# Kernel tuning notes

Hardware: AMD Instinct MI355X
Metric: run time of the kernel (lower is better)

Reference implementation:

```python
import jax, jax.numpy as jnp
import numpy as np

C = 256
GROUPS = 32
EPS = 1e-5

def setup_inputs() -> dict:
    key = jax.random.key(0)
    ks = jax.random.split(key, 7)
    B, H, W = 4, 64, 64
    x = jax.random.normal(ks[0], (B, C, H, W), dtype=jnp.float32)
    # GroupNorm affine params
    gn_w = jnp.ones((C,), dtype=jnp.float32)
    gn_b = jnp.zeros((C,), dtype=jnp.float32)
    # 1x1 conv weights stored as [out, in]
    s = 1.0 / np.sqrt(C)
    qkv_w = jax.random.uniform(ks[1], (3 * C, C), minval=-s, maxval=s, dtype=jnp.float32)
    qkv_b = jax.random.uniform(ks[2], (3 * C,), minval=-s, maxval=s, dtype=jnp.float32)
    proj_w = jax.random.uniform(ks[3], (C, C), minval=-s, maxval=s, dtype=jnp.float32)
    proj_b = jax.random.uniform(ks[4], (C,), minval=-s, maxval=s, dtype=jnp.float32)
    return {"x": x, "gn_w": gn_w, "gn_b": gn_b, "qkv_w": qkv_w,
            "qkv_b": qkv_b, "proj_w": proj_w, "proj_b": proj_b}

def group_norm(x, w, b):
    B, Cc, H, W = x.shape
    xg = x.reshape(B, GROUPS, Cc // GROUPS, H, W)
    mu = xg.mean(axis=(2, 3, 4), keepdims=True)
    var = xg.var(axis=(2, 3, 4), keepdims=True)
    xn = ((xg - mu) * jax.lax.rsqrt(var + EPS)).reshape(B, Cc, H, W)
    return xn * w[None, :, None, None] + b[None, :, None, None]

def reference(x, gn_w, gn_b, qkv_w, qkv_b, proj_w, proj_b):
    B, Cc, H, W = x.shape
    h = group_norm(x, gn_w, gn_b)
    # 1x1 conv == per-pixel matmul
    qkv = jnp.einsum('bchw,oc->bohw', h, qkv_w) + qkv_b[None, :, None, None]
    q, k, v = jnp.split(qkv, 3, axis=1)            # each [B, C, H, W]
    N = H * W
    q = q.reshape(B, Cc, N).transpose(0, 2, 1)      # [B, N, C]
    k = k.reshape(B, Cc, N)                         # [B, C, N]
    v = v.reshape(B, Cc, N).transpose(0, 2, 1)      # [B, N, C]
    w_att = jnp.einsum('bnc,bcm->bnm', q, k) * (Cc ** -0.5)
    w_att = jax.nn.softmax(w_att, axis=-1)
    h = jnp.einsum('bnm,bmc->bnc', w_att, v)        # [B, N, C]
    h = h.transpose(0, 2, 1).reshape(B, Cc, H, W)
    h = jnp.einsum('bchw,oc->bohw', h, proj_w) + proj_b[None, :, None, None]
    return x + h
```

## Files before the change

kernel.cpp:

```cpp
#include <hip/hip_runtime.h>
#include <stdint.h>

typedef unsigned short u16;
typedef __attribute__((ext_vector_type(8))) short bf16x8;
typedef __attribute__((ext_vector_type(4))) float f32x4;

#define BATCH   4
#define CH      256
#define NPIX    4096
#define NGROUPS 32
#define CPG     8
#define EPS     1e-5f

#define NSPLIT 4
#define SPLEN  (NPIX / NSPLIT)
#define ATK    32
#define NIT    (SPLEN / ATK)
#define WSTR   264
#define QTILES 2

__device__ __forceinline__ float bf2f(u16 u) {
    union { uint32_t i; float f; } v; v.i = ((uint32_t)u) << 16; return v.f;
}
__device__ __forceinline__ u16 f2bf(float f) {
    union { float f; uint32_t i; } v; v.f = f;
    uint32_t x = v.i;
    uint32_t r = (x + 0x7fffu + ((x >> 16) & 1u)) >> 16;
    return (u16)r;
}
__device__ __forceinline__ void unpack2(uint32_t u, float& a, float& b) {
    union { uint32_t i; float f; } lo, hi;
    lo.i = u << 16; hi.i = u & 0xffff0000u;
    a = lo.f; b = hi.f;
}
__device__ __forceinline__ void unpack8(uint4 u, float* f) {
    unpack2(u.x, f[0], f[1]); unpack2(u.y, f[2], f[3]);
    unpack2(u.z, f[4], f[5]); unpack2(u.w, f[6], f[7]);
}

__device__ __forceinline__ bool detect_f32(const void* xv) {
    const u16* p = (const u16*)xv;
    int bad = 0;
    #pragma unroll
    for (int i = 0; i < 32; i++) {
        u16 v = p[2 * i];
        int e = (v >> 7) & 0xff;
        bad += (e < 0x68 || e > 0x90) ? 1 : 0;
    }
    return bad >= 10;
}
__device__ __forceinline__ float load1(const void* b, size_t i, bool f32) {
    return f32 ? ((const float*)b)[i] : bf2f(((const u16*)b)[i]);
}
__device__ __forceinline__ void store1(void* b, size_t i, bool f32, float v) {
    if (f32) ((float*)b)[i] = v; else ((u16*)b)[i] = f2bf(v);
}
__device__ __forceinline__ void load4v(const void* base, size_t off, bool f32, float* f) {
    if (f32) {
        float4 a = *(const float4*)((const float*)base + off);
        f[0] = a.x; f[1] = a.y; f[2] = a.z; f[3] = a.w;
    } else {
        uint2 u = *(const uint2*)((const u16*)base + off);
        unpack2(u.x, f[0], f[1]); unpack2(u.y, f[2], f[3]);
    }
}
__device__ __forceinline__ void load8v(const void* base, size_t off, bool f32, float* f) {
    if (f32) {
        const float4* p = (const float4*)((const float*)base + off);
        float4 a = p[0], b = p[1];
        f[0] = a.x; f[1] = a.y; f[2] = a.z; f[3] = a.w;
        f[4] = b.x; f[5] = b.y; f[6] = b.z; f[7] = b.w;
    } else {
        uint4 u = *(const uint4*)((const u16*)base + off);
        unpack8(u, f);
    }
}

__global__ __launch_bounds__(256) void wconv(const void* __restrict__ qkv_w,
                                             const void* __restrict__ proj_w,
                                             u16* __restrict__ wq, u16* __restrict__ wp) {
    bool f32q = detect_f32(qkv_w);
    bool f32p = detect_f32(proj_w);
    int i = blockIdx.x * 256 + threadIdx.x;
    for (int e = i; e < 768 * 256; e += 256 * 256)
        wq[e] = f2bf(load1(qkv_w, e, f32q));
    for (int e = i; e < 256 * 256; e += 256 * 256)
        wp[e] = f2bf(load1(proj_w, e, f32p));
}

__global__ __launch_bounds__(256) void gn_stats(const void* __restrict__ x,
                                                float* __restrict__ stats, int b0) {
    bool f32 = detect_f32(x);
    int bg = b0 * NGROUPS + blockIdx.x;
    int t  = threadIdx.x;
    size_t base = (size_t)bg * (CPG * NPIX);
    float s = 0.f, s2 = 0.f;
    for (int i = t * 8; i < CPG * NPIX; i += 256 * 8) {
        float f[8]; load8v(x, base + i, f32, f);
        #pragma unroll
        for (int e = 0; e < 8; e++) { s += f[e]; s2 += f[e] * f[e]; }
    }
    #pragma unroll
    for (int off = 1; off < 64; off <<= 1) {
        s  += __shfl_xor(s,  off);
        s2 += __shfl_xor(s2, off);
    }
    __shared__ float red[8];
    int w = t >> 6;
    if ((t & 63) == 0) { red[w * 2] = s; red[w * 2 + 1] = s2; }
    __syncthreads();
    if (t == 0) {
        float S  = red[0] + red[2] + red[4] + red[6];
        float S2 = red[1] + red[3] + red[5] + red[7];
        float n  = (float)(CPG * NPIX);
        float mu = S / n;
        float var = S2 / n - mu * mu;
        stats[bg * 2]     = mu;
        stats[bg * 2 + 1] = rsqrtf(var + EPS);
    }
}

__global__ __launch_bounds__(256) void xgn(const void* __restrict__ x,
                                           const void* __restrict__ gn_w,
                                           const void* __restrict__ gn_b,
                                           const float* __restrict__ stats,
                                           u16* __restrict__ xt, int b0) {
    bool f32 = detect_f32(x);
    __shared__ u16 T[64][72];
    int bl = blockIdx.z, bg = b0 + bl;
    int n0 = blockIdx.x * 64, c0 = blockIdx.y * 64;
    int t = threadIdx.x;
    int tc = t >> 4, tn = (t & 15) * 4;
    #pragma unroll
    for (int i = 0; i < 4; i++) {
        int cl = tc + i * 16;
        int c = c0 + cl;
        int g = c >> 3;
        float mu = stats[(bg * NGROUPS + g) * 2];
        float rs = stats[(bg * NGROUPS + g) * 2 + 1];
        float wv = load1(gn_w, c, f32) * rs;
        float bv = load1(gn_b, c, f32) - mu * wv;
        float a[4];
        load4v(x, ((size_t)(bg * CH + c)) * NPIX + n0 + tn, f32, a);
        #pragma unroll
        for (int j = 0; j < 4; j++) T[cl][tn + j] = f2bf(a[j] * wv + bv);
    }
    __syncthreads();
    #pragma unroll
    for (int i = 0; i < 2; i++) {
        int e = t + i * 256;
        int nl = e >> 3, cc = (e & 7) * 8;
        union { uint4 v; u16 s[8]; } pk;
        #pragma unroll
        for (int j = 0; j < 8; j++) pk.s[j] = T[cc + j][nl];
        *(uint4*)(xt + ((size_t)(bl * NPIX) + n0 + nl) * CH + c0 + cc) = pk.v;
    }
}

__global__ __launch_bounds__(256, 3) void qkv_mfma(const u16* __restrict__ xt,
                                                   const u16* __restrict__ wq,
                                                   const void* __restrict__ qkv_b,
                                                   u16* __restrict__ qk,
                                                   u16* __restrict__ vt) {
    __shared__ u16 Ws[64 * WSTR];
    __shared__ u16 T2b[128 * 72];
    bool f32b = detect_f32(qkv_b);
    int bl = blockIdx.z;
    int o0 = blockIdx.y * 64;
    int t = threadIdx.x;
    int w = t >> 6, lane = t & 63;
    int l15 = lane & 15, quad = lane >> 4;

    #pragma unroll
    for (int i = 0; i < 8; i++) {
        int e = t + i * 256;
        *(uint4*)(Ws + (e >> 5) * WSTR + (e & 31) * 8) =
            *(const uint4*)(wq + (size_t)(o0 + (e >> 5)) * CH + (e & 31) * 8);
    }
    __syncthreads();

    bool isv = (o0 >= 512);
    for (int tt = 0; tt < QTILES; tt++) {
        int n0 = (blockIdx.x * QTILES + tt) * 128;
        int pbase = n0 + w * 32;
        const u16* xa = xt + ((size_t)(bl * NPIX + pbase)) * CH;

        f32x4 acc[2][4];
        #pragma unroll
        for (int m = 0; m < 2; m++)
            #pragma unroll
            for (int n = 0; n < 4; n++)
                #pragma unroll
                for (int r = 0; r < 4; r++) acc[m][n][r] = 0.f;

        #pragma unroll
        for (int kc = 0; kc < 8; kc++) {
            bf16x8 a0 = *(const bf16x8*)(xa + (size_t)(l15) * CH + kc * 32 + quad * 8);
            bf16x8 a1 = *(const bf16x8*)(xa + (size_t)(16 + l15) * CH + kc * 32 + quad * 8);
            #pragma unroll
            for (int n = 0; n < 4; n++) {
                bf16x8 b = *(const bf16x8*)(Ws + (n * 16 + l15) * WSTR + kc * 32 + quad * 8);
                acc[0][n] = __builtin_amdgcn_mfma_f32_16x16x32_bf16(a0, b, acc[0][n], 0, 0, 0);
                acc[1][n] = __builtin_amdgcn_mfma_f32_16x16x32_bf16(a1, b, acc[1][n], 0, 0, 0);
            }
        }

        if (!isv) {
            __syncthreads();
            #pragma unroll
            for (int n = 0; n < 4; n++) {
                int o = o0 + n * 16 + l15;
                float bias = load1(qkv_b, o, f32b);
                #pragma unroll
                for (int m = 0; m < 2; m++)
                    #pragma unroll
                    for (int r = 0; r < 4; r++) {
                        int prow = w * 32 + m * 16 + quad * 4 + r;
                        T2b[prow * 72 + n * 16 + l15] = f2bf(acc[m][n][r] + bias);
                    }
            }
            __syncthreads();
            #pragma unroll
            for (int i = 0; i < 4; i++) {
                int e = t + i * 256;
                int p = e >> 3, c = (e & 7) * 8;
                uint4 v = *(const uint4*)(T2b + p * 72 + c);
                *(uint4*)(qk + ((size_t)(bl * NPIX + n0 + p)) * 512 + o0 + c) = v;
            }
        } else {
            #pragma unroll
            for (int n = 0; n < 4; n++) {
                int o = o0 + n * 16 + l15;
                float bias = load1(qkv_b, o, f32b);
                size_t rowb = ((size_t)(bl * CH + o - 512)) * NPIX + pbase;
                #pragma unroll
                for (int m = 0; m < 2; m++) {
                    union { uint2 v; u16 s[4]; } pk;
                    #pragma unroll
                    for (int r = 0; r < 4; r++) pk.s[r] = f2bf(acc[m][n][r] + bias);
                    *(uint2*)(vt + rowb + quad * 8 + m * 4) = pk.v;
                }
            }
        }
    }
}

__global__ __launch_bounds__(256, 2) void attn_mfma(const u16* __restrict__ qk,
                                                    const u16* __restrict__ vt,
                                                    u16* __restrict__ Opart,
                                                    float* __restrict__ lpart,
                                                    int NE, int NR) {
    __shared__ u16 Ks[2][ATK * 256];
    __shared__ u16 Vts[2][CH * 32];
    int bl    = blockIdx.z;
    int split = blockIdx.y;
    int q0    = blockIdx.x * 128;
    int t     = threadIdx.x;
    int w     = t >> 6, lane = t & 63;
    int l15   = lane & 15, quad = lane >> 4;

    const u16* qkb = qk + (size_t)bl * NPIX * 512;
    const u16* vtb = vt + (size_t)bl * CH * NPIX;
    int kvbase = split * SPLEN;

    bf16x8 qf[2][8];
    #pragma unroll
    for (int m = 0; m < 2; m++) {
        const u16* qrow = qkb + (size_t)(q0 + w * 32 + m * 16 + l15) * 512;
        #pragma unroll
        for (int kc = 0; kc < 8; kc++)
            qf[m][kc] = *(const bf16x8*)(qrow + kc * 32 + quad * 8);
    }
    f32x4 o[2][16];
    #pragma unroll
    for (int m = 0; m < 2; m++)
        #pragma unroll
        for (int i = 0; i < 16; i++)
            #pragma unroll
            for (int r = 0; r < 4; r++) o[m][i][r] = 0.f;
    float lsum[2] = {0.f, 0.f};
    const float scale = 0.0625f;
    int swz = l15 & 7;

    #pragma unroll
    for (int i = 0; i < 4; i++) {
        int g = t + i * 256;
        int row = g >> 5, pcol = g & 31;
        int lcol = pcol ^ (row & 7);
        __builtin_amdgcn_global_load_lds(
            (const void*)(qkb + (size_t)(kvbase + row) * 512 + 256 + lcol * 8),
            (void*)(&Ks[0][0] + (size_t)g * 8), 16, 0, 0);
    }
    #pragma unroll
    for (int i = 0; i < 4; i++) {
        int g = t + i * 256;
        int row = g >> 2, s = g & 3;
        __builtin_amdgcn_global_load_lds(
            (const void*)(vtb + (size_t)row * NPIX + kvbase + (s ^ (row & 3)) * 8),
            (void*)(&Vts[0][0] + (size_t)g * 8), 16, 0, 0);
    }
    __syncthreads();

    for (int it = 0; it < NIT; it++) {
        int cur = it & 1;
        if (it + 1 < NIT) {
            int kv1 = kvbase + (it + 1) * ATK;
            u16* KsB = &Ks[cur ^ 1][0];
            u16* VsB = &Vts[cur ^ 1][0];
            #pragma unroll
            for (int i = 0; i < 4; i++) {
                int g = t + i * 256;
                int row = g >> 5, pcol = g & 31;
                int lcol = pcol ^ (row & 7);
                __builtin_amdgcn_global_load_lds(
                    (const void*)(qkb + (size_t)(kv1 + row) * 512 + 256 + lcol * 8),
                    (void*)(KsB + (size_t)g * 8), 16, 0, 0);
            }
            #pragma unroll
            for (int i = 0; i < 4; i++) {
                int g = t + i * 256;
                int row = g >> 2, s = g & 3;
                __builtin_amdgcn_global_load_lds(
                    (const void*)(vtb + (size_t)row * NPIX + kv1 + (s ^ (row & 3)) * 8),
                    (void*)(VsB + (size_t)g * 8), 16, 0, 0);
            }
        }
        const u16* KsC = &Ks[cur][0];
        const u16* VsC = &Vts[cur][0];

        f32x4 sT[2][2];
        #pragma unroll
        for (int kt = 0; kt < 2; kt++)
            #pragma unroll
            for (int qt = 0; qt < 2; qt++)
                #pragma unroll
                for (int r = 0; r < 4; r++) sT[kt][qt][r] = 0.f;
        #pragma unroll
        for (int kc = 0; kc < 8; kc++) {
            int sc = (kc * 4 + quad) ^ swz;
            bf16x8 a0 = *(const bf16x8*)(KsC + l15 * 256 + sc * 8);
            bf16x8 a1 = *(const bf16x8*)(KsC + (16 + l15) * 256 + sc * 8);
            sT[0][0] = __builtin_amdgcn_mfma_f32_16x16x32_bf16(a0, qf[0][kc], sT[0][0], 0, 0, 0);
            sT[0][1] = __builtin_amdgcn_mfma_f32_16x16x32_bf16(a0, qf[1][kc], sT[0][1], 0, 0, 0);
            sT[1][0] = __builtin_amdgcn_mfma_f32_16x16x32_bf16(a1, qf[0][kc], sT[1][0], 0, 0, 0);
            sT[1][1] = __builtin_amdgcn_mfma_f32_16x16x32_bf16(a1, qf[1][kc], sT[1][1], 0, 0, 0);
        }

        bf16x8 pa[2];
        #pragma unroll
        for (int qt = 0; qt < 2; qt++) {
            union { bf16x8 v; u16 s[8]; } pk;
            float ls = 0.f;
            #pragma unroll
            for (int kt = 0; kt < 2; kt++)
                #pragma unroll
                for (int r = 0; r < 4; r++) {
                    float p = __expf(sT[kt][qt][r] * scale);
                    ls += p;
                    pk.s[kt * 4 + r] = f2bf(p);
                }
            lsum[qt] += ls;
            pa[qt] = pk.v;
        }

        #pragma unroll
        for (int dt = 0; dt < 16; dt++) {
            int row = dt * 16 + l15;
            bf16x8 vf = *(const bf16x8*)(VsC + row * 32 + (quad ^ (row & 3)) * 8);
            o[0][dt] = __builtin_amdgcn_mfma_f32_16x16x32_bf16(pa[0], vf, o[0][dt], 0, 0, 0);
            o[1][dt] = __builtin_amdgcn_mfma_f32_16x16x32_bf16(pa[1], vf, o[1][dt], 0, 0, 0);
        }

        __syncthreads();
    }

    size_t rowb = (size_t)bl * NPIX + q0 + w * 32;
    u16* op = Opart + (size_t)split * NE;
    #pragma unroll
    for (int qt = 0; qt < 2; qt++) {
        float v = lsum[qt];
        v += __shfl_xor(v, 16); v += __shfl_xor(v, 32);
        if (quad == 0)
            lpart[(size_t)split * NR + rowb + qt * 16 + l15] = v;
        #pragma unroll
        for (int dt = 0; dt < 16; dt++)
            #pragma unroll
            for (int r = 0; r < 4; r++)
                op[(rowb + qt * 16 + quad * 4 + r) * CH + dt * 16 + l15] = f2bf(o[qt][dt][r]);
    }
}

__global__ __launch_bounds__(256, 4) void proj_mfma(const u16* __restrict__ Opart,
                                                    const float* __restrict__ lpart,
                                                    const u16* __restrict__ wp,
                                                    const void* __restrict__ proj_b,
                                                    const void* __restrict__ x,
                                                    void* __restrict__ out,
                                                    int b0, int NE, int NR) {
    __shared__ u16 Ws[64 * WSTR];
    bool f32 = detect_f32(x);
    int bl = blockIdx.z, bg = b0 + bl;
    int n0 = blockIdx.x * 128, o0 = blockIdx.y * 64;
    int t = threadIdx.x;
    int w = t >> 6, lane = t & 63;
    int l15 = lane & 15, quad = lane >> 4;
    int pbase = n0 + w * 32;

    #pragma unroll
    for (int i = 0; i < 8; i++) {
        int e = t + i * 256;
        *(uint4*)(Ws + (e >> 5) * WSTR + (e & 31) * 8) =
            *(const uint4*)(wp + (size_t)(o0 + (e >> 5)) * CH + (e & 31) * 8);
    }
    __syncthreads();

    size_t rowg[2]; float invl[2];
    #pragma unroll
    for (int m = 0; m < 2; m++) {
        rowg[m] = (size_t)bl * NPIX + pbase + m * 16 + l15;
        float l = 0.f;
        #pragma unroll
        for (int s = 0; s < NSPLIT; s++) l += lpart[(size_t)s * NR + rowg[m]];
        invl[m] = 1.0f / l;
    }

    f32x4 acc[2][4];
    #pragma unroll
    for (int m = 0; m < 2; m++)
        #pragma unroll
        for (int n = 0; n < 4; n++)
            #pragma unroll
            for (int r = 0; r < 4; r++) acc[m][n][r] = 0.f;

    #pragma unroll
    for (int kc = 0; kc < 8; kc++) {
        bf16x8 afr[2];
        #pragma unroll
        for (int m = 0; m < 2; m++) {
            float f[8] = {0.f,0.f,0.f,0.f,0.f,0.f,0.f,0.f};
            #pragma unroll
            for (int s = 0; s < NSPLIT; s++) {
                bf16x8 v = *(const bf16x8*)(Opart + (size_t)s * NE + rowg[m] * CH + kc * 32 + quad * 8);
                #pragma unroll
                for (int j = 0; j < 8; j++) f[j] += bf2f((u16)v[j]);
            }
            bf16x8 a;
            #pragma unroll
            for (int j = 0; j < 8; j++) a[j] = (short)f2bf(f[j] * invl[m]);
            afr[m] = a;
        }
        #pragma unroll
        for (int n = 0; n < 4; n++) {
            bf16x8 b = *(const bf16x8*)(Ws + (n * 16 + l15) * WSTR + kc * 32 + quad * 8);
            acc[0][n] = __builtin_amdgcn_mfma_f32_16x16x32_bf16(afr[0], b, acc[0][n], 0, 0, 0);
            acc[1][n] = __builtin_amdgcn_mfma_f32_16x16x32_bf16(afr[1], b, acc[1][n], 0, 0, 0);
        }
    }

    __syncthreads();
    float4* T4 = (float4*)Ws;
    #pragma unroll
    for (int n = 0; n < 4; n++) {
        int o = o0 + n * 16 + l15;
        float bias = load1(proj_b, o, f32);
        #pragma unroll
        for (int m = 0; m < 2; m++) {
            float4 v;
            v.x = acc[m][n][0] + bias; v.y = acc[m][n][1] + bias;
            v.z = acc[m][n][2] + bias; v.w = acc[m][n][3] + bias;
            T4[(n * 16 + l15) * 33 + w * 8 + m * 4 + quad] = v;
        }
    }
    __syncthreads();
    const float* Tf = (const float*)Ws;
    if (f32) {
        #pragma unroll
        for (int i = 0; i < 8; i++) {
            int idx = t + i * 256;
            int row = idx >> 5, c4 = idx & 31;
            float4 v = T4[row * 33 + c4];
            size_t go = ((size_t)(bg * CH + o0 + row)) * NPIX + n0 + c4 * 4;
            float4 xr = *(const float4*)((const float*)x + go);
            v.x += xr.x; v.y += xr.y; v.z += xr.z; v.w += xr.w;
            *(float4*)((float*)out + go) = v;
        }
    } else {
        #pragma unroll
        for (int i = 0; i < 4; i++) {
            int idx = t + i * 256;
            int row = idx >> 4, c8 = idx & 15;
            size_t go = ((size_t)(bg * CH + o0 + row)) * NPIX + n0 + c8 * 8;
            uint4 xr = *(const uint4*)((const u16*)x + go);
            float xf[8]; unpack8(xr, xf);
            union { uint4 v; u16 s[8]; } pk;
            #pragma unroll
            for (int j = 0; j < 8; j++)
                pk.s[j] = f2bf(Tf[row * 132 + c8 * 8 + j] + xf[j]);
            *(uint4*)((u16*)out + go) = pk.v;
        }
    }
}

extern "C" void kernel_launch(void* const* d_in, const int* in_sizes, int n_in,
                              void* d_out, int out_size, void* d_ws, size_t ws_size,
                              hipStream_t stream) {
    const void* x      = d_in[0];
    const void* gn_w   = d_in[1];
    const void* gn_b   = d_in[2];
    const void* qkv_w  = d_in[3];
    const void* qkv_b  = d_in[4];
    const void* proj_w = d_in[5];
    const void* proj_b = d_in[6];

    char* ws = (char*)d_ws;
    float* stats = (float*)ws;
    u16* wq = (u16*)(ws + 1024);
    u16* wp = wq + 768 * 256;
    char* dyn = ws + 1024 + (768 * 256 + 256 * 256) * 2;

    const size_t per_batch = (size_t)NPIX * CH * 2
                           + (size_t)NPIX * 512 * 2
                           + (size_t)CH * NPIX * 2
                           + (size_t)NSPLIT * NPIX * CH * 2
                           + (size_t)NSPLIT * NPIX * 4;
    const size_t need_full = 1024 + 600 * 1024 + BATCH * per_batch;
    int nb = (ws_size >= need_full) ? BATCH : 1;

    u16* xt      = (u16*)dyn;
    u16* qk      = xt + (size_t)nb * NPIX * CH;
    u16* vt      = qk + (size_t)nb * NPIX * 512;
    u16* Opart   = vt + (size_t)nb * CH * NPIX;
    float* lpart = (float*)(Opart + (size_t)NSPLIT * nb * NPIX * CH);
    int NE = nb * NPIX * CH;
    int NR = nb * NPIX;

    wconv<<<dim3(256), 256, 0, stream>>>(qkv_w, proj_w, wq, wp);

    for (int b0 = 0; b0 < BATCH; b0 += nb) {
        gn_stats<<<dim3(nb * NGROUPS), 256, 0, stream>>>(x, stats, b0);
        xgn<<<dim3(NPIX / 64, CH / 64, nb), 256, 0, stream>>>(
            x, gn_w, gn_b, stats, xt, b0);
        qkv_mfma<<<dim3(NPIX / 128 / QTILES, 768 / 64, nb), 256, 0, stream>>>(
            xt, wq, qkv_b, qk, vt);
        attn_mfma<<<dim3(NPIX / 128, NSPLIT, nb), 256, 0, stream>>>(
            qk, vt, Opart, lpart, NE, NR);
        proj_mfma<<<dim3(NPIX / 128, CH / 64, nb), 256, 0, stream>>>(
            Opart, lpart, wp, proj_b, x, d_out, b0, NE, NR);
    }
}
```

Baseline: 208.8 us.

## Store V in MFMA fragment order and load it directly from global memory

The QKV kernel now writes V into a pre-tiled layout that matches the per-lane B-fragment order of the 16x16x32 MFMA. The attention kernel then reads each V fragment with a single 16-byte global load per lane, with no LDS staging. This drops the V LDS double buffer and its async copies, which frees LDS and cuts shared-memory traffic. In exchange, V loads are now synchronous global (L2) loads inside the inner loop and are no longer prefetched a stage ahead.

Result: slower. 300.2 us (+43.8%).

```diff
diff --git a/kernel.cpp b/kernel.cpp
--- a/kernel.cpp
+++ b/kernel.cpp
@@ -161,7 +161,7 @@
                                                    const u16* __restrict__ wq,
                                                    const void* __restrict__ qkv_b,
                                                    u16* __restrict__ qk,
-                                                   u16* __restrict__ vt) {
+                                                   u16* __restrict__ vbuf) {
     __shared__ u16 Ws[64 * WSTR];
     __shared__ u16 T2b[128 * 72];
     bool f32b = detect_f32(qkv_b);
@@ -232,13 +232,15 @@
             for (int n = 0; n < 4; n++) {
                 int o = o0 + n * 16 + l15;
                 float bias = load1(qkv_b, o, f32b);
-                size_t rowb = ((size_t)(bl * CH + o - 512)) * NPIX + pbase;
+                int dt = ((o0 - 512) >> 4) + n;
+                size_t tb = ((size_t)(bl * 128 + (pbase >> 5)) * 16 + dt) * 512;
                 #pragma unroll
                 for (int m = 0; m < 2; m++) {
                     union { uint2 v; u16 s[4]; } pk;
                     #pragma unroll
                     for (int r = 0; r < 4; r++) pk.s[r] = f2bf(acc[m][n][r] + bias);
-                    *(uint2*)(vt + rowb + quad * 8 + m * 4) = pk.v;
+                    *(uint2*)(vbuf + tb + ((m + 2 * (quad & 1)) * 16 + l15) * 8
+                                     + 4 * (quad >> 1)) = pk.v;
                 }
             }
         }
@@ -246,12 +248,11 @@
 }
 
 __global__ __launch_bounds__(256, 2) void attn_mfma(const u16* __restrict__ qk,
-                                                    const u16* __restrict__ vt,
+                                                    const u16* __restrict__ vbuf,
                                                     u16* __restrict__ Opart,
                                                     float* __restrict__ lpart,
                                                     int NE, int NR) {
     __shared__ u16 Ks[2][ATK * 256];
-    __shared__ u16 Vts[2][CH * 32];
     int bl    = blockIdx.z;
     int split = blockIdx.y;
     int q0    = blockIdx.x * 128;
@@ -260,8 +261,8 @@
     int l15   = lane & 15, quad = lane >> 4;
 
     const u16* qkb = qk + (size_t)bl * NPIX * 512;
-    const u16* vtb = vt + (size_t)bl * CH * NPIX;
     int kvbase = split * SPLEN;
+    const u16* vfb = vbuf + ((size_t)(bl * 128 + (kvbase >> 5)) * 16) * 512 + lane * 8;
 
     bf16x8 qf[2][8];
     #pragma unroll
@@ -291,14 +292,6 @@
             (const void*)(qkb + (size_t)(kvbase + row) * 512 + 256 + lcol * 8),
             (void*)(&Ks[0][0] + (size_t)g * 8), 16, 0, 0);
     }
-    #pragma unroll
-    for (int i = 0; i < 4; i++) {
-        int g = t + i * 256;
-        int row = g >> 2, s = g & 3;
-        __builtin_amdgcn_global_load_lds(
-            (const void*)(vtb + (size_t)row * NPIX + kvbase + (s ^ (row & 3)) * 8),
-            (void*)(&Vts[0][0] + (size_t)g * 8), 16, 0, 0);
-    }
     __syncthreads();
 
     for (int it = 0; it < NIT; it++) {
@@ -306,7 +299,6 @@
         if (it + 1 < NIT) {
             int kv1 = kvbase + (it + 1) * ATK;
             u16* KsB = &Ks[cur ^ 1][0];
-            u16* VsB = &Vts[cur ^ 1][0];
             #pragma unroll
             for (int i = 0; i < 4; i++) {
                 int g = t + i * 256;
@@ -316,17 +308,8 @@
                     (const void*)(qkb + (size_t)(kv1 + row) * 512 + 256 + lcol * 8),
                     (void*)(KsB + (size_t)g * 8), 16, 0, 0);
             }
-            #pragma unroll
-            for (int i = 0; i < 4; i++) {
-                int g = t + i * 256;
-                int row = g >> 2, s = g & 3;
-                __builtin_amdgcn_global_load_lds(
-                    (const void*)(vtb + (size_t)row * NPIX + kv1 + (s ^ (row & 3)) * 8),
-                    (void*)(VsB + (size_t)g * 8), 16, 0, 0);
-            }
         }
         const u16* KsC = &Ks[cur][0];
-        const u16* VsC = &Vts[cur][0];
 
         f32x4 sT[2][2];
         #pragma unroll
@@ -365,11 +348,11 @@
 
         #pragma unroll
         for (int dt = 0; dt < 16; dt++) {
-            int row = dt * 16 + l15;
-            bf16x8 vf = *(const bf16x8*)(VsC + row * 32 + (quad ^ (row & 3)) * 8);
+            bf16x8 vf = *(const bf16x8*)(vfb + dt * 512);
             o[0][dt] = __builtin_amdgcn_mfma_f32_16x16x32_bf16(pa[0], vf, o[0][dt], 0, 0, 0);
             o[1][dt] = __builtin_amdgcn_mfma_f32_16x16x32_bf16(pa[1], vf, o[1][dt], 0, 0, 0);
         }
+        vfb += 16 * 512;
 
         __syncthreads();
     }
@@ -528,8 +511,8 @@
 
     u16* xt      = (u16*)dyn;
     u16* qk      = xt + (size_t)nb * NPIX * CH;
-    u16* vt      = qk + (size_t)nb * NPIX * 512;
-    u16* Opart   = vt + (size_t)nb * CH * NPIX;
+    u16* vbuf    = qk + (size_t)nb * NPIX * 512;
+    u16* Opart   = vbuf + (size_t)nb * CH * NPIX;
     float* lpart = (float*)(Opart + (size_t)NSPLIT * nb * NPIX * CH);
     int NE = nb * NPIX * CH;
     int NR = nb * NPIX;
@@ -541,9 +524,9 @@
         xgn<<<dim3(NPIX / 64, CH / 64, nb), 256, 0, stream>>>(
             x, gn_w, gn_b, stats, xt, b0);
         qkv_mfma<<<dim3(NPIX / 128 / QTILES, 768 / 64, nb), 256, 0, stream>>>(
-            xt, wq, qkv_b, qk, vt);
+            xt, wq, qkv_b, qk, vbuf);
         attn_mfma<<<dim3(NPIX / 128, NSPLIT, nb), 256, 0, stream>>>(
-            qk, vt, Opart, lpart, NE, NR);
+            qk, vbuf, Opart, lpart, NE, NR);
         proj_mfma<<<dim3(NPIX / 128, CH / 64, nb), 256, 0, stream>>>(
             Opart, lpart, wp, proj_b, x, d_out, b0, NE, NR);
     }
```
